# Optimization experiments

Hardware: AMD Instinct MI355X
Metric: run time of the kernel (lower is better)

Reference implementation:

```python
import jax, jax.numpy as jnp
import numpy as np
import math

B, P, N, D = 64, 96, 12, 2048
W = P - N + 1  # 85 sliding windows
SCALE = 1.0 / math.sqrt(2048.0)
LN_EPS = 1e-5


def setup_inputs() -> dict:
    key = jax.random.key(0)
    ks = jax.random.split(key, 16)
    g = lambda k, shape: (jax.random.normal(k, shape, dtype=jnp.float32) * 0.02)
    return {
        "fc_feats": jax.random.normal(ks[0], (B, P, D), dtype=jnp.float32),
        "nsa_q_w": g(ks[1], (D, D)), "nsa_q_b": jnp.zeros((D,), jnp.float32),
        "nsa_k_w": g(ks[2], (D, D)), "nsa_k_b": jnp.zeros((D,), jnp.float32),
        "nsa_v_w": g(ks[3], (D, D)), "nsa_v_b": jnp.zeros((D,), jnp.float32),
        "nsa_fc_w": g(ks[4], (N, N)), "nsa_fc_b": jnp.zeros((N,), jnp.float32),
        "ds_w": g(ks[5], (W, P)), "ds_b": jnp.zeros((W,), jnp.float32),
        "ln_g": jnp.ones((D,), jnp.float32), "ln_b": jnp.zeros((D,), jnp.float32),
        "sa_q_w": g(ks[6], (D, D)), "sa_q_b": jnp.zeros((D,), jnp.float32),
        "sa_k_w": g(ks[7], (D, D)), "sa_k_b": jnp.zeros((D,), jnp.float32),
        "sa_v_w": g(ks[8], (D, D)), "sa_v_b": jnp.zeros((D,), jnp.float32),
        "sa_fc_w": g(ks[9], (W, W)), "sa_fc_b": jnp.zeros((W,), jnp.float32),
    }


def _encoder(fc_feats, nsa_q_w, nsa_q_b, nsa_k_w, nsa_k_b, nsa_v_w, nsa_v_b,
             nsa_fc_w, nsa_fc_b, ds_w, ds_b, ln_g, ln_b,
             sa_q_w, sa_q_b, sa_k_w, sa_k_b, sa_v_w, sa_v_b, sa_fc_w, sa_fc_b):
    # ---- Neighboring self-attention over all W sliding windows at once ----
    idx = jnp.arange(W)[:, None] + jnp.arange(N)[None, :]      # [W, N]
    win = fc_feats[:, idx, :]                                  # [B, W, N, D]
    q = jnp.einsum('bwnd,ed->bwne', win, nsa_q_w) + nsa_q_b
    k = jnp.einsum('bwnd,ed->bwne', win, nsa_k_w) + nsa_k_b
    v = jnp.einsum('bwnd,ed->bwne', win, nsa_v_w) + nsa_v_b
    attn = jax.nn.softmax(jnp.einsum('bwne,bwme->bwnm', q, k) * SCALE, axis=-1)
    nf = jnp.einsum('bwnm,bwmd->bwnd', attn, v)                # [B, W, N, D]
    # mask is a constant ones buffer [B,1,N] fed through fc + softmax
    mask = jnp.ones((B, N), jnp.float32)
    wmask = jax.nn.softmax(mask @ nsa_fc_w.T + nsa_fc_b, axis=-1)  # [B, N]
    nsa_feats = jnp.einsum('bn,bwnd->bwd', wmask, nf)          # [B, W, D]

    # ---- downsample over the image axis: Linear(P -> W) ----
    new_fc = jnp.einsum('bpd,wp->bwd', fc_feats, ds_w) + ds_b[None, :, None]

    # ---- residual + LayerNorm over D ----
    x = new_fc + nsa_feats
    mu = jnp.mean(x, axis=-1, keepdims=True)
    var = jnp.mean(jnp.square(x - mu), axis=-1, keepdims=True)
    x = (x - mu) * jax.lax.rsqrt(var + LN_EPS) * ln_g + ln_b   # [B, W, D]

    # ---- global self-attention over the W positions ----
    q2 = jnp.einsum('bwd,ed->bwe', x, sa_q_w) + sa_q_b
    k2 = jnp.einsum('bwd,ed->bwe', x, sa_k_w) + sa_k_b
    v2 = jnp.einsum('bwd,ed->bwe', x, sa_v_w) + sa_v_b
    attn2 = jax.nn.softmax(jnp.einsum('bwe,bue->bwu', q2, k2) * SCALE, axis=-1)
    nf2 = jnp.einsum('bwu,bud->bwd', attn2, v2)                # [B, W, D]
    mask2 = jnp.ones((B, W), jnp.float32)
    wmask2 = jax.nn.softmax(mask2 @ sa_fc_w.T + sa_fc_b, axis=-1)  # [B, W]
    return jnp.einsum('bw,bwd->bd', wmask2, nf2)               # [B, D]


def reference(fc_feats, nsa_q_w, nsa_q_b, nsa_k_w, nsa_k_b, nsa_v_w, nsa_v_b,
              nsa_fc_w, nsa_fc_b, ds_w, ds_b, ln_g, ln_b,
              sa_q_w, sa_q_b, sa_k_w, sa_k_b, sa_v_w, sa_v_b, sa_fc_w, sa_fc_b):
    return _encoder(fc_feats, nsa_q_w, nsa_q_b, nsa_k_w, nsa_k_b, nsa_v_w, nsa_v_b,
                    nsa_fc_w, nsa_fc_b, ds_w, ds_b, ln_g, ln_b,
                    sa_q_w, sa_q_b, sa_k_w, sa_k_b, sa_v_w, sa_v_b, sa_fc_w, sa_fc_b)
```

## Files before the change

kernel.cpp:

```cpp
#include <hip/hip_runtime.h>
#include <hip/hip_bf16.h>

#define DEV __device__ __forceinline__

typedef __attribute__((ext_vector_type(8))) short s16x8;
typedef __attribute__((ext_vector_type(4))) float f32x4;

#define B_ 64
#define P_ 96
#define N_ 12
#define D_ 2048
#define W_ 85
#define M1_ (B_ * P_)
#define M2_ (B_ * W_)
#define M2P_ 5504
#define SCALE_F 0.02209708691207961f
#define LN_EPS_F 1e-5f

DEV float b2f(short h) { return __uint_as_float(((unsigned)(unsigned short)h) << 16); }
DEV short f2b(float f) {
  __hip_bfloat16 h = __float2bfloat16(f);
  return *reinterpret_cast<short*>(&h);
}

DEV void gload_lds16(const void* g, void* l) {
  __builtin_amdgcn_global_load_lds(
      (const __attribute__((address_space(1))) unsigned int*)(unsigned long long)g,
      (__attribute__((address_space(3))) unsigned int*)(unsigned int)(unsigned long long)l,
      16, 0, 0);
}

__global__ __launch_bounds__(256) void castA_kernel(const float* s, short* d, int n) {
  const int i = (blockIdx.x * 256 + threadIdx.x) * 8;
  if (i >= n) return;
  float4 a = *(const float4*)(s + i);
  float4 b = *(const float4*)(s + i + 4);
  s16x8 o;
  o[0] = f2b(a.x); o[1] = f2b(a.y); o[2] = f2b(a.z); o[3] = f2b(a.w);
  o[4] = f2b(b.x); o[5] = f2b(b.y); o[6] = f2b(b.z); o[7] = f2b(b.w);
  *(s16x8*)(d + i) = o;
}

struct Cast2 { const float* s[2]; short* d[2]; };

__global__ __launch_bounds__(256) void cast2_kernel(Cast2 j, int n) {
  const int jb = blockIdx.y;
  const int i = (blockIdx.x * 256 + threadIdx.x) * 8;
  if (i >= n) return;
  const float* src = j.s[jb] + i;
  float4 a = *(const float4*)(src);
  float4 b = *(const float4*)(src + 4);
  s16x8 o;
  o[0] = f2b(a.x); o[1] = f2b(a.y); o[2] = f2b(a.z); o[3] = f2b(a.w);
  o[4] = f2b(b.x); o[5] = f2b(b.y); o[6] = f2b(b.z); o[7] = f2b(b.w);
  *(s16x8*)(j.d[jb] + i) = o;
}

struct Cast4T { const float* s[4]; short* d[4]; };

__global__ __launch_bounds__(256) void castT_kernel(Cast4T j) {
  __shared__ float tl[64][65];
  const int z = blockIdx.z;
  const float* src = j.s[z];
  short* dst = j.d[z];
  const int e0 = blockIdx.x * 64, d0 = blockIdx.y * 64;
  const int t = threadIdx.x;
  for (int i = t; i < 64 * 16; i += 256) {
    const int er = i >> 4, c4 = (i & 15) * 4;
    const float4 v = *(const float4*)(src + (long)(e0 + er) * 2048 + d0 + c4);
    tl[c4 + 0][er] = v.x;
    tl[c4 + 1][er] = v.y;
    tl[c4 + 2][er] = v.z;
    tl[c4 + 3][er] = v.w;
  }
  __syncthreads();
  for (int i = t; i < 64 * 8; i += 256) {
    const int dr = i >> 3, e8 = (i & 7) * 8;
    s16x8 o;
#pragma unroll
    for (int e = 0; e < 8; ++e) o[e] = f2b(tl[dr][e8 + e]);
    *(s16x8*)(dst + (long)(d0 + dr) * 2048 + e0 + e8) = o;
  }
}

__global__ __launch_bounds__(256) void prep_kernel(const float* nw, const float* nb,
                                                   const float* sw, const float* sb, float* wm,
                                                   const float* wk1, const float* bq1, float* r1,
                                                   const float* wk2, const float* bq2, float* r2) {
  const int bx = blockIdx.x, t = threadIdx.x;
  if (bx == 0) {
    __shared__ float l1[12], l2[85];
    if (t < 12) { float s = nb[t]; for (int n = 0; n < 12; ++n) s += nw[t * 12 + n]; l1[t] = s; }
    if (t < 85) { float s = sb[t]; for (int w = 0; w < 85; ++w) s += sw[t * 85 + w]; l2[t] = s; }
    __syncthreads();
    if (t == 0) {
      float m = l1[0]; for (int i = 1; i < 12; ++i) m = fmaxf(m, l1[i]);
      float s = 0.f; float e[12];
      for (int i = 0; i < 12; ++i) { e[i] = expf(l1[i] - m); s += e[i]; }
      for (int i = 0; i < 12; ++i) wm[i] = e[i] / s;
    } else if (t == 64) {
      float m = l2[0]; for (int i = 1; i < 85; ++i) m = fmaxf(m, l2[i]);
      float s = 0.f;
      for (int i = 0; i < 85; ++i) s += expf(l2[i] - m);
      for (int i = 0; i < 85; ++i) wm[16 + i] = expf(l2[i] - m) / s;
    }
    return;
  }
  const int idx = bx - 1;
  const int stage = idx >> 6;
  const int ec = (idx & 63) >> 3, dpc = idx & 7;
  const float* wk = stage ? wk2 : wk1;
  const float* bq = stage ? bq2 : bq1;
  float* r = stage ? r2 : r1;
  const int dp = dpc * 256 + t;
  const int e0 = ec * 256;
  float s = 0.f;
  for (int e = e0; e < e0 + 256; ++e) s += bq[e] * wk[(long)e * 2048 + dp];
  atomicAdd(&r[dp], s);
}

struct GemmArgs {
  const short* A[3];
  const short* Wt[3];
  const float* bias[3];
  void* C[3];
  int mlim;
};

template <int OM>
__global__ __launch_bounds__(256) void gemm_nt_bf16(GemmArgs g) {
  __shared__ short As[2][4096];
  __shared__ short Bs[2][4096];
  const int z = blockIdx.z;
  const short* A = g.A[z];
  const short* Wm = g.Wt[z];
  const int tid = threadIdx.x, wave = tid >> 6, lane = tid & 63;
  const int wmo = (wave >> 1) * 64, wno = (wave & 1) * 64;
  const long rowA0 = (long)blockIdx.x * 128;
  const long rowB0 = (long)blockIdx.y * 128;
  const int kg = lane >> 4, rsub = lane & 15;

  f32x4 acc[4][4];
  const f32x4 zz = {0.f, 0.f, 0.f, 0.f};
#pragma unroll
  for (int i = 0; i < 4; ++i)
#pragma unroll
    for (int jj = 0; jj < 4; ++jj) acc[i][jj] = zz;

  auto stage = [&](int bb, int kbase) {
#pragma unroll
    for (int i = 0; i < 2; ++i) {
      const int row = i * 64 + lane;
      gload_lds16(A + (rowA0 + row) * 2048 + kbase + wave * 8,
                  (char*)As[bb] + (wave * 128 + i * 64) * 16);
      gload_lds16(Wm + (rowB0 + row) * 2048 + kbase + wave * 8,
                  (char*)Bs[bb] + (wave * 128 + i * 64) * 16);
    }
  };

  stage(0, 0);
  __syncthreads();
  for (int kt = 0; kt < 64; ++kt) {
    const int cur = kt & 1;
    if (kt < 63) stage(cur ^ 1, (kt + 1) * 32);
    s16x8 af[4], bv[4];
#pragma unroll
    for (int f = 0; f < 4; ++f) {
      af[f] = *(const s16x8*)(As[cur] + (kg * 128 + wmo + f * 16 + rsub) * 8);
      bv[f] = *(const s16x8*)(Bs[cur] + (kg * 128 + wno + f * 16 + rsub) * 8);
    }
#pragma unroll
    for (int i = 0; i < 4; ++i)
#pragma unroll
      for (int jj = 0; jj < 4; ++jj)
        acc[i][jj] = __builtin_amdgcn_mfma_f32_16x16x32_bf16(af[i], bv[jj], acc[i][jj], 0, 0, 0);
    __syncthreads();
  }

  const float* bias = g.bias[z];
#pragma unroll
  for (int i = 0; i < 4; ++i) {
    const long row = rowA0 + wmo + i * 16 + (lane >> 4) * 4;
#pragma unroll
    for (int jj = 0; jj < 4; ++jj) {
      const long col = rowB0 + wno + jj * 16 + (lane & 15);
      const float bvl = bias ? bias[col] : 0.f;
#pragma unroll
      for (int r = 0; r < 4; ++r) {
        if (row + r < g.mlim) {
          if (OM == 0)
            ((short*)g.C[z])[(row + r) * 2048 + col] = f2b(acc[i][jj][r] + bvl);
          else
            ((float*)g.C[z])[(row + r) * 2048 + col] = acc[i][jj][r] + bvl;
        }
      }
    }
  }
}

__global__ __launch_bounds__(256) void out_gemm_kernel(const short* A, const short* Wm,
                                                       const float* bias, float* C) {
  __shared__ short As[2][4][64][8];
  __shared__ short Bs[2][4][128][8];
  const int kz = blockIdx.x;
  const long rowB0 = (long)blockIdx.y * 128;
  const int tid = threadIdx.x, wave = tid >> 6, lane = tid & 63;
  const int wno = wave * 32;
  const int kgx = lane >> 4, rsub = lane & 15;

  f32x4 acc[4][2];
  const f32x4 zz = {0.f, 0.f, 0.f, 0.f};
#pragma unroll
  for (int f = 0; f < 4; ++f) { acc[f][0] = zz; acc[f][1] = zz; }

  auto stage = [&](int bb, int kbase) {
    gload_lds16(A + (long)lane * 2048 + kbase + wave * 8, (char*)As[bb] + tid * 16);
#pragma unroll
    for (int i = 0; i < 2; ++i) {
      const int row = i * 64 + lane;
      gload_lds16(Wm + (rowB0 + row) * 2048 + kbase + wave * 8,
                  (char*)Bs[bb] + (wave * 128 + i * 64) * 16);
    }
  };

  const int kb0 = kz * 512;
  stage(0, kb0);
  __syncthreads();
  for (int kt = 0; kt < 16; ++kt) {
    const int cur = kt & 1;
    if (kt < 15) stage(cur ^ 1, kb0 + (kt + 1) * 32);
    s16x8 af[4], bv[2];
#pragma unroll
    for (int f = 0; f < 4; ++f) af[f] = *(const s16x8*)&As[cur][kgx][f * 16 + rsub][0];
#pragma unroll
    for (int j = 0; j < 2; ++j) bv[j] = *(const s16x8*)&Bs[cur][kgx][wno + j * 16 + rsub][0];
#pragma unroll
    for (int f = 0; f < 4; ++f)
#pragma unroll
      for (int j = 0; j < 2; ++j)
        acc[f][j] = __builtin_amdgcn_mfma_f32_16x16x32_bf16(af[f], bv[j], acc[f][j], 0, 0, 0);
    __syncthreads();
  }

#pragma unroll
  for (int f = 0; f < 4; ++f) {
    const int row = f * 16 + (lane >> 4) * 4;
#pragma unroll
    for (int j = 0; j < 2; ++j) {
      const long col = rowB0 + wno + j * 16 + (lane & 15);
      const float bvl = (kz == 0) ? bias[col] : 0.f;
#pragma unroll
      for (int r = 0; r < 4; ++r)
        atomicAdd(&C[(long)(row + r) * 2048 + col], acc[f][j][r] + bvl);
    }
  }
}

template <int STAGE>
__global__ __launch_bounds__(256) void attn_mfma_kernel(const short* Aq, const short* Bk,
                                                        const float* wm, float* outp) {
  __shared__ short As[2][8][96][8];
  __shared__ short Bs[2][8][96][8];
  __shared__ float S[96][97];
  __shared__ float C1[85][12];
  __shared__ float M1[85][12];
  const int b = blockIdx.x;
  const int tid = threadIdx.x, wave = tid >> 6, lane = tid & 63;
  const int RPB = (STAGE == 1) ? 96 : 85;
  const long base = (long)b * RPB * 2048;
  const int wr0 = (wave >> 1) * 48, wc0 = (wave & 1) * 48;
  const int fr = lane & 15, fk = lane >> 4;

  f32x4 acc[3][3];
  const f32x4 zz = {0.f, 0.f, 0.f, 0.f};
#pragma unroll
  for (int i = 0; i < 3; ++i)
#pragma unroll
    for (int j = 0; j < 3; ++j) acc[i][j] = zz;

  auto stage = [&](int bb, int kb) {
#pragma unroll
    for (int it = 0; it < 3; ++it) {
      const int u = it * 256 + tid;
      const int row = u % 96, kg = u / 96;
      gload_lds16(Aq + base + (long)row * 2048 + kb + kg * 8, (char*)As[bb] + u * 16);
      gload_lds16(Bk + base + (long)row * 2048 + kb + kg * 8, (char*)Bs[bb] + u * 16);
    }
  };

  stage(0, 0);
  __syncthreads();
  for (int kt = 0; kt < 32; ++kt) {
    const int cur = kt & 1;
    if (kt < 31) stage(cur ^ 1, (kt + 1) * 64);
#pragma unroll
    for (int ks = 0; ks < 2; ++ks) {
      const int kgx = ks * 4 + fk;
      s16x8 af[3], bv[3];
#pragma unroll
      for (int i = 0; i < 3; ++i) {
        af[i] = *(const s16x8*)&As[cur][kgx][wr0 + i * 16 + fr][0];
        bv[i] = *(const s16x8*)&Bs[cur][kgx][wc0 + i * 16 + fr][0];
      }
#pragma unroll
      for (int i = 0; i < 3; ++i)
#pragma unroll
        for (int j = 0; j < 3; ++j)
          acc[i][j] = __builtin_amdgcn_mfma_f32_16x16x32_bf16(af[i], bv[j], acc[i][j], 0, 0, 0);
    }
    __syncthreads();
  }
#pragma unroll
  for (int i = 0; i < 3; ++i)
#pragma unroll
    for (int j = 0; j < 3; ++j)
#pragma unroll
      for (int r = 0; r < 4; ++r)
        S[wr0 + i * 16 + fk * 4 + r][wc0 + j * 16 + fr] = acc[i][j][r];
  __syncthreads();

  if (STAGE == 2) {
    if (tid < 85) {
      float mx = -1e30f;
      for (int u = 0; u < 85; ++u) mx = fmaxf(mx, S[tid][u]);
      float sum = 0.f;
      for (int u = 0; u < 85; ++u) {
        const float e = expf((S[tid][u] - mx) * SCALE_F);
        S[tid][u] = e;
        sum += e;
      }
      (&C1[0][0])[tid] = wm[tid] / sum;
    }
    __syncthreads();
    if (tid < 85) {
      float a = 0.f;
      for (int i = 0; i < 85; ++i) a += (&C1[0][0])[i] * S[i][tid];
      outp[b * 85 + tid] = a;
    }
  } else {
    for (int p = tid; p < 85 * 12; p += 256) {
      const int w = p / 12, n = p % 12;
      const int row = w + n;
      float mx = -1e30f;
      for (int m = 0; m < 12; ++m) mx = fmaxf(mx, S[row][w + m]);
      float sum = 0.f;
      for (int m = 0; m < 12; ++m) sum += expf((S[row][w + m] - mx) * SCALE_F);
      M1[w][n] = mx;
      C1[w][n] = wm[n] / sum;
    }
    __syncthreads();
    for (int p = tid; p < 85 * 12; p += 256) {
      const int w = p / 12, m = p % 12;
      float a = 0.f;
#pragma unroll
      for (int n = 0; n < 12; ++n)
        a += C1[w][n] * expf((S[w + n][w + m] - M1[w][n]) * SCALE_F);
      outp[(b * 85 + w) * 12 + m] = a;
    }
  }
}

__global__ __launch_bounds__(256) void combine_kernel(const float* fc32, const short* vp,
                                                      const float* p1, const float* dsw_g,
                                                      const float* dsb, float* X) {
  const int b = blockIdx.y, d0 = blockIdx.x * 128;
  const int t = threadIdx.x;
  __shared__ float fcs[96][128];
  __shared__ short vps[96][128];
  __shared__ float dsw[85][96];
  __shared__ float p1s[85][12];
  for (int s = t; s < 96 * 32; s += 256) {
    const int row = s >> 5, c4 = (s & 31) * 4;
    *(float4*)&fcs[row][c4] = *(const float4*)(fc32 + ((long)b * 96 + row) * 2048 + d0 + c4);
  }
  for (int s = t; s < 96 * 16; s += 256) {
    const int row = s >> 4, c8 = (s & 15) * 8;
    *(s16x8*)&vps[row][c8] = *(const s16x8*)(vp + ((long)b * 96 + row) * 2048 + d0 + c8);
  }
  for (int s = t; s < 85 * 96; s += 256) (&dsw[0][0])[s] = dsw_g[s];
  for (int s = t; s < 85 * 12; s += 256) (&p1s[0][0])[s] = p1[(long)b * 85 * 12 + s];
  __syncthreads();
  const int dp = (t & 63) * 2, wslot = t >> 6;
  for (int w = wslot; w < 85; w += 4) {
    float a0 = dsb[w], a1 = a0;
    for (int p = 0; p < 96; ++p) {
      const float c = dsw[w][p];
      a0 += c * fcs[p][dp];
      a1 += c * fcs[p][dp + 1];
    }
#pragma unroll
    for (int m = 0; m < 12; ++m) {
      const unsigned vv = *(const unsigned*)&vps[w + m][dp];
      const float c = p1s[w][m];
      a0 += c * __uint_as_float(vv << 16);
      a1 += c * __uint_as_float(vv & 0xffff0000u);
    }
    const long o = ((long)b * 85 + w) * 2048 + d0 + dp;
    X[o] = a0;
    X[o + 1] = a1;
  }
}

__global__ __launch_bounds__(256) void ln_kernel(const float* X, const float* gam,
                                                 const float* bet, short* XLN) {
  const long row = blockIdx.x;
  const int t = threadIdx.x;
  float v[8];
  *(float4*)&v[0] = *(const float4*)(X + row * 2048 + t * 8);
  *(float4*)&v[4] = *(const float4*)(X + row * 2048 + t * 8 + 4);
  float s = 0.f, q = 0.f;
#pragma unroll
  for (int e = 0; e < 8; ++e) { s += v[e]; q += v[e] * v[e]; }
#pragma unroll
  for (int o = 32; o > 0; o >>= 1) { s += __shfl_down(s, o); q += __shfl_down(q, o); }
  __shared__ float rs[4], rq[4];
  if ((t & 63) == 0) { rs[t >> 6] = s; rq[t >> 6] = q; }
  __syncthreads();
  const float S = rs[0] + rs[1] + rs[2] + rs[3];
  const float Q = rq[0] + rq[1] + rq[2] + rq[3];
  const float mu = S * (1.f / 2048.f);
  const float var = Q * (1.f / 2048.f) - mu * mu;
  const float rstd = rsqrtf(var + LN_EPS_F);
  s16x8 o8;
#pragma unroll
  for (int e = 0; e < 8; ++e) {
    const int c = t * 8 + e;
    o8[e] = f2b((v[e] - mu) * rstd * gam[c] + bet[c]);
  }
  *(s16x8*)(XLN + row * 2048 + t * 8) = o8;
}

__global__ __launch_bounds__(256) void z2_kernel(const short* xln, const float* p2, short* z2) {
  const int b = blockIdx.y, d = blockIdx.x * 256 + threadIdx.x;
  __shared__ float pc[85];
  if (threadIdx.x < 85) pc[threadIdx.x] = p2[b * 85 + threadIdx.x];
  __syncthreads();
  float a = 0.f;
  for (int u = 0; u < 85; ++u) a += pc[u] * b2f(xln[((long)b * 85 + u) * 2048 + d]);
  z2[(long)b * 2048 + d] = f2b(a);
}

extern "C" void kernel_launch(void* const* d_in, const int* in_sizes, int n_in,
                              void* d_out, int out_size, void* d_ws, size_t ws_size,
                              hipStream_t stream) {
  char* ws = (char*)d_ws;
  size_t off = 0;
  auto alloc = [&](size_t bytes) -> char* {
    char* p = ws + off;
    off += (bytes + 255) & ~(size_t)255;
    return p;
  };

  short* A1   = (short*)alloc((size_t)M1_ * D_ * 2);
  short* WqT1 = (short*)alloc((size_t)D_ * D_ * 2);
  short* WkT1 = (short*)alloc((size_t)D_ * D_ * 2);
  short* WqT2 = (short*)alloc((size_t)D_ * D_ * 2);
  short* WkT2 = (short*)alloc((size_t)D_ * D_ * 2);
  short* Gt1  = (short*)alloc((size_t)D_ * D_ * 2);
  short* Gt2  = (short*)alloc((size_t)D_ * D_ * 2);
  short* Wv1c = (short*)alloc((size_t)D_ * D_ * 2);
  short* Wv2c = (short*)alloc((size_t)D_ * D_ * 2);
  short* Y1   = (short*)alloc((size_t)M1_ * D_ * 2);
  short* VP   = (short*)alloc((size_t)M1_ * D_ * 2);
  float* X    = (float*)alloc((size_t)M2_ * D_ * 4);
  float* P1   = (float*)alloc((size_t)B_ * W_ * N_ * 4);
  short* Z2   = (short*)alloc((size_t)64 * D_ * 2);
  float* P2   = (float*)alloc((size_t)B_ * W_ * 4);
  float* WM   = (float*)alloc(512);
  float* R1   = (float*)alloc(D_ * 4);
  float* R2   = (float*)alloc(D_ * 4);

  short* XLN = A1;
  short* Y2  = Y1;

  if (off > ws_size) return;

  const size_t zbytes = (size_t)((char*)R2 - (char*)P2) + D_ * 4;
  hipMemsetAsync(P2, 0, zbytes, stream);
  hipMemsetAsync(d_out, 0, (size_t)B_ * D_ * 4, stream);

  castA_kernel<<<dim3(6144), 256, 0, stream>>>((const float*)d_in[0], A1, M1_ * D_);
  Cast4T ct;
  ct.s[0] = (const float*)d_in[1];  ct.d[0] = WqT1;
  ct.s[1] = (const float*)d_in[3];  ct.d[1] = WkT1;
  ct.s[2] = (const float*)d_in[13]; ct.d[2] = WqT2;
  ct.s[3] = (const float*)d_in[15]; ct.d[3] = WkT2;
  castT_kernel<<<dim3(32, 32, 4), 256, 0, stream>>>(ct);
  Cast2 cv;
  cv.s[0] = (const float*)d_in[5];  cv.d[0] = Wv1c;
  cv.s[1] = (const float*)d_in[17]; cv.d[1] = Wv2c;
  cast2_kernel<<<dim3(2048, 2), 256, 0, stream>>>(cv, D_ * D_);
  prep_kernel<<<dim3(129), 256, 0, stream>>>(
      (const float*)d_in[7], (const float*)d_in[8],
      (const float*)d_in[19], (const float*)d_in[20], WM,
      (const float*)d_in[3], (const float*)d_in[2], R1,
      (const float*)d_in[15], (const float*)d_in[14], R2);

  GemmArgs gg;
  gg.A[0] = WkT1; gg.Wt[0] = WqT1; gg.bias[0] = nullptr; gg.C[0] = Gt1;
  gg.A[1] = WkT2; gg.Wt[1] = WqT2; gg.bias[1] = nullptr; gg.C[1] = Gt2;
  gg.mlim = 2048;
  gemm_nt_bf16<0><<<dim3(16, 16, 2), 256, 0, stream>>>(gg);

  GemmArgs g1;
  g1.A[0] = A1; g1.Wt[0] = Wv1c; g1.bias[0] = (const float*)d_in[6]; g1.C[0] = VP;
  g1.A[1] = A1; g1.Wt[1] = Gt1;  g1.bias[1] = R1;                    g1.C[1] = Y1;
  g1.mlim = M1_;
  gemm_nt_bf16<0><<<dim3(48, 16, 2), 256, 0, stream>>>(g1);

  attn_mfma_kernel<1><<<dim3(64), 256, 0, stream>>>(Y1, A1, WM, P1);

  combine_kernel<<<dim3(16, 64), 256, 0, stream>>>((const float*)d_in[0], VP, P1,
                                                   (const float*)d_in[9],
                                                   (const float*)d_in[10], X);
  ln_kernel<<<dim3(5440), 256, 0, stream>>>(X, (const float*)d_in[11], (const float*)d_in[12], XLN);

  GemmArgs g2;
  g2.A[0] = XLN; g2.Wt[0] = Gt2; g2.bias[0] = R2; g2.C[0] = Y2;
  g2.mlim = M2P_;
  gemm_nt_bf16<0><<<dim3(43, 16, 1), 256, 0, stream>>>(g2);

  attn_mfma_kernel<2><<<dim3(64), 256, 0, stream>>>(Y2, XLN, WM + 16, P2);

  z2_kernel<<<dim3(8, 64), 256, 0, stream>>>(XLN, P2, Z2);

  out_gemm_kernel<<<dim3(4, 16), 256, 0, stream>>>(Z2, Wv2c, (const float*)d_in[18],
                                                   (float*)d_out);
}
```

Before: 841.7 us.

## Prefetch two K-tiles ahead in GEMM with counted vmcnt waits

Restructures the bf16 GEMM main loop so two stages are in flight. Each iteration waits only for the older stage's global-to-LDS loads via vmcnt(4), reads fragments into registers, then barriers and reissues the next load into the buffer just consumed, before running the MFMAs. Per-row pointers are precomputed to cut address arithmetic. This aims to hide global load latency behind compute, at the cost of relying on hand-placed waitcnt and barrier ordering.

```diff
diff --git a/kernel.cpp b/kernel.cpp
--- a/kernel.cpp
+++ b/kernel.cpp
@@ -140,6 +140,11 @@
   const long rowB0 = (long)blockIdx.y * 128;
   const int kg = lane >> 4, rsub = lane & 15;
 
+  const short* pA0 = A + (rowA0 + lane) * 2048 + wave * 8;
+  const short* pA1 = pA0 + 64 * 2048;
+  const short* pB0 = Wm + (rowB0 + lane) * 2048 + wave * 8;
+  const short* pB1 = pB0 + 64 * 2048;
+
   f32x4 acc[4][4];
   const f32x4 zz = {0.f, 0.f, 0.f, 0.f};
 #pragma unroll
@@ -147,34 +152,39 @@
 #pragma unroll
     for (int jj = 0; jj < 4; ++jj) acc[i][jj] = zz;
 
-  auto stage = [&](int bb, int kbase) {
-#pragma unroll
-    for (int i = 0; i < 2; ++i) {
-      const int row = i * 64 + lane;
-      gload_lds16(A + (rowA0 + row) * 2048 + kbase + wave * 8,
-                  (char*)As[bb] + (wave * 128 + i * 64) * 16);
-      gload_lds16(Wm + (rowB0 + row) * 2048 + kbase + wave * 8,
-                  (char*)Bs[bb] + (wave * 128 + i * 64) * 16);
-    }
+  auto stage = [&](int bb, int kt2) {
+    const int kb = kt2 * 32;
+    gload_lds16(pA0 + kb, (char*)As[bb] + (wave * 128) * 16);
+    gload_lds16(pA1 + kb, (char*)As[bb] + (wave * 128 + 64) * 16);
+    gload_lds16(pB0 + kb, (char*)Bs[bb] + (wave * 128) * 16);
+    gload_lds16(pB1 + kb, (char*)Bs[bb] + (wave * 128 + 64) * 16);
   };
 
   stage(0, 0);
-  __syncthreads();
+  stage(1, 1);
   for (int kt = 0; kt < 64; ++kt) {
     const int cur = kt & 1;
-    if (kt < 63) stage(cur ^ 1, (kt + 1) * 32);
+    if (kt < 63) {
+      asm volatile("s_waitcnt vmcnt(4)" ::: "memory");
+    } else {
+      asm volatile("s_waitcnt vmcnt(0)" ::: "memory");
+    }
+    __builtin_amdgcn_s_barrier();
     s16x8 af[4], bv[4];
 #pragma unroll
     for (int f = 0; f < 4; ++f) {
       af[f] = *(const s16x8*)(As[cur] + (kg * 128 + wmo + f * 16 + rsub) * 8);
       bv[f] = *(const s16x8*)(Bs[cur] + (kg * 128 + wno + f * 16 + rsub) * 8);
     }
+    asm volatile("s_waitcnt lgkmcnt(0)" ::: "memory");
+    __builtin_amdgcn_sched_barrier(0);
+    __builtin_amdgcn_s_barrier();
+    if (kt < 62) stage(cur, kt + 2);
 #pragma unroll
     for (int i = 0; i < 4; ++i)
 #pragma unroll
       for (int jj = 0; jj < 4; ++jj)
         acc[i][jj] = __builtin_amdgcn_mfma_f32_16x16x32_bf16(af[i], bv[jj], acc[i][jj], 0, 0, 0);
-    __syncthreads();
   }
 
   const float* bias = g.bias[z];
```

New measurement: 815.1 us. 1.03x faster.
